# Kernel optimization log

Measured on AMD Instinct MI355X. Metric: run time of the kernel, lower is better.

## Reference

```python
import jax, jax.numpy as jnp
import numpy as np

N = 50000
V = 3
DIM = 128
H = 64


def setup_inputs() -> dict:
    key = jax.random.key(0)
    ks = jax.random.split(key, 8)
    x = jax.random.normal(ks[0], (N, V * DIM), dtype=jnp.float32)
    edge_index = jax.random.randint(ks[1], (2, 800000), 0, N, dtype=jnp.int64)
    Wv = jax.random.normal(ks[2], (V, DIM, H), dtype=jnp.float32) * (1.0 / np.sqrt(DIM))
    bv = jnp.zeros((V, H), dtype=jnp.float32)
    na_w = jax.random.normal(ks[3], (H, 1), dtype=jnp.float32) * (1.0 / np.sqrt(H))
    na_b = jnp.zeros((1,), dtype=jnp.float32)
    va_w1 = jax.random.normal(ks[4], (H, H // 2), dtype=jnp.float32) * (1.0 / np.sqrt(H))
    va_b1 = jnp.zeros((H // 2,), dtype=jnp.float32)
    va_w2 = jax.random.normal(ks[5], (H // 2, 1), dtype=jnp.float32) * (1.0 / np.sqrt(H // 2))
    va_b2 = jnp.zeros((1,), dtype=jnp.float32)
    cls_w = jax.random.normal(ks[6], (H, 2), dtype=jnp.float32) * (1.0 / np.sqrt(H))
    cls_b = jnp.zeros((2,), dtype=jnp.float32)
    return dict(x=x, edge_index=edge_index, Wv=Wv, bv=bv, na_w=na_w, na_b=na_b,
                va_w1=va_w1, va_b1=va_b1, va_w2=va_w2, va_b2=va_b2,
                cls_w=cls_w, cls_b=cls_b)


def reference(x, edge_index, Wv, bv, na_w, na_b, va_w1, va_b1, va_w2, va_b2, cls_w, cls_b):
    n = x.shape[0]
    # split into equal-dim views: [N, V, DIM]
    xv = x.reshape(n, V, DIM)

    # --- GCNConv (PyG defaults): linear transform, add self-loops, sym-norm aggregate, bias ---
    h = jnp.einsum('nvd,vdh->nvh', xv, Wv)  # [N, V, H]

    src = edge_index[0]
    dst = edge_index[1]
    loop = jnp.arange(n, dtype=src.dtype)
    src_full = jnp.concatenate([src, loop])
    dst_full = jnp.concatenate([dst, loop])

    ones = jnp.ones(src_full.shape[0], dtype=h.dtype)
    deg = jax.ops.segment_sum(ones, dst_full, num_segments=n)  # in-degree incl. self-loop
    dinv = jnp.where(deg > 0, 1.0 / jnp.sqrt(deg), 0.0)
    norm = dinv[src_full] * dinv[dst_full]  # [E+N]

    msgs = h[src_full] * norm[:, None, None]            # [E+N, V, H]
    agg = jax.ops.segment_sum(msgs, dst_full, num_segments=n)  # [N, V, H]
    agg = agg + bv[None, :, :]

    # ReLU
    emb = jax.nn.relu(agg)  # [N, V, H]

    # --- NodeAttentionLayer: softmax over nodes (dim=0), applied per view ---
    scores = jnp.einsum('nvh,ho->nvo', emb, na_w) + na_b  # [N, V, 1]
    att = jax.nn.softmax(scores, axis=0)
    emb_w = emb * att  # [N, V, H]

    # --- ViewAttention ---
    avg = jnp.mean(emb_w, axis=0)  # [V, H]
    vs = jnp.tanh(avg @ va_w1 + va_b1) @ va_w2 + va_b2  # [V, 1]
    vw = jax.nn.softmax(vs.T, axis=1)  # [1, V]
    fused = jnp.einsum('nvh,v->nh', emb_w, vw[0])  # [N, H]

    # --- classifier + log_softmax ---
    logits = fused @ cls_w + cls_b
    logp = jax.nn.log_softmax(logits, axis=1)
    return logp, fused, vw[0]
```

## Files before the change

### kernel.cpp

```cpp
#include <hip/hip_runtime.h>
#include <math.h>

#define NV 3
#define DIMX 128
#define HD 64
#define NVH 192
#define NBLK 256
#define NBUK 128
#define BSH 9

typedef unsigned int uint32;
typedef unsigned short ushort16;
typedef unsigned char uchar;
typedef __attribute__((ext_vector_type(8))) short short8;
typedef __attribute__((ext_vector_type(4))) float f32x4;

__device__ __forceinline__ unsigned fkey(float f){
  unsigned b = __float_as_uint(f);
  return (b & 0x80000000u) ? ~b : (b | 0x80000000u);
}
__device__ __forceinline__ float unkey(unsigned k){
  return __uint_as_float((k & 0x80000000u) ? (k ^ 0x80000000u) : ~k);
}
__device__ __forceinline__ uint32 bf16rne(float f){
  uint32 u = __float_as_uint(f);
  return (u + 0x7fffu + ((u >> 16) & 1u)) >> 16;
}
__device__ __forceinline__ float bfus(uint32 q){ return __uint_as_float(q << 16); }

__global__ void k_zero(float* __restrict__ wsum, float* __restrict__ sumexp, unsigned* __restrict__ maxkey){
  int t = threadIdx.x;
  if (t < NVH) wsum[t] = 0.f;
  else if (t < NVH+3) sumexp[t-NVH] = 0.f;
  else if (t < NVH+6) maxkey[t-NVH-3] = 0u;
}

__global__ __launch_bounds__(256) void k_hist(const int* __restrict__ ei, int E, int EPB,
                                              int* __restrict__ histT){
  __shared__ int sh[NBUK];
  int t = threadIdx.x, b = blockIdx.x;
  if (t < NBUK) sh[t] = 0;
  __syncthreads();
  int e0 = b*EPB, e1 = min(e0 + EPB, E);
  for (int i = e0 + t; i < e1; i += 256){
    int d = ei[E + i];
    atomicAdd(&sh[d >> BSH], 1);
  }
  __syncthreads();
  if (t < NBUK) histT[t*NBLK + b] = sh[t];
}

__global__ __launch_bounds__(1024) void k_hscan(int* __restrict__ histT){
  __shared__ int sh[1024];
  int t = threadIdx.x;
  int lo = t*32;
  int vals[32]; int s = 0;
  #pragma unroll
  for (int k = 0; k < 32; ++k){ vals[k] = histT[lo+k]; s += vals[k]; }
  sh[t] = s; __syncthreads();
  for (int ofs = 1; ofs < 1024; ofs <<= 1){
    int v = (t >= ofs) ? sh[t-ofs] : 0;
    __syncthreads();
    sh[t] += v;
    __syncthreads();
  }
  int run = sh[t] - s;
  #pragma unroll
  for (int k = 0; k < 32; ++k){ histT[lo+k] = run; run += vals[k]; }
}

__global__ __launch_bounds__(256) void k_scatter(const int* __restrict__ ei, int E, int EPB,
                                                 const int* __restrict__ ofsT, uint32* __restrict__ ebuf){
  __shared__ int cur[NBUK];
  int t = threadIdx.x, b = blockIdx.x;
  if (t < NBUK) cur[t] = ofsT[t*NBLK + b];
  __syncthreads();
  int e0 = b*EPB, e1 = min(e0 + EPB, E);
  for (int i = e0 + t; i < e1; i += 256){
    int s = ei[i], d = ei[E + i];
    int pos = atomicAdd(&cur[d >> BSH], 1);
    ebuf[pos] = ((uint32)(d & 511) << 16) | (uint32)s;
  }
}

__global__ __launch_bounds__(512) void k_csr(const uint32* __restrict__ ebuf, const int* __restrict__ ofsT,
                                             int E, int N, int* __restrict__ rowstart,
                                             float* __restrict__ dinv, int* __restrict__ csr){
  __shared__ int cnt[512];
  __shared__ int pre[512];
  int t = threadIdx.x, b = blockIdx.x;
  int estart = ofsT[b*NBLK];
  int eend   = ((b+1)*NBLK < NBUK*NBLK) ? ofsT[(b+1)*NBLK] : E;
  int n0 = b << BSH;
  int nn = min(512, N - n0);
  cnt[t] = 0;
  __syncthreads();
  for (int i = estart + t; i < eend; i += 512){
    atomicAdd(&cnt[ebuf[i] >> 16], 1);
  }
  __syncthreads();
  int c = cnt[t];
  pre[t] = c;
  __syncthreads();
  for (int ofs = 1; ofs < 512; ofs <<= 1){
    int v = (t >= ofs) ? pre[t-ofs] : 0;
    __syncthreads();
    pre[t] += v;
    __syncthreads();
  }
  int excl = pre[t] - c;
  if (t < nn){
    rowstart[n0 + t] = estart + excl;
    dinv[n0 + t] = rsqrtf((float)(c + 1));
  }
  if (b == gridDim.x - 1 && t == 0) rowstart[N] = E;
  cnt[t] = estart + excl;
  __syncthreads();
  for (int i = estart + t; i < eend; i += 512){
    uint32 e = ebuf[i];
    int pos = atomicAdd(&cnt[e >> 16], 1);
    csr[pos] = (int)(e & 0xFFFFu);
  }
}

__global__ __launch_bounds__(256) void k_wpack(const float* __restrict__ Wv, uint32* __restrict__ Wb){
  int t = blockIdx.x*blockDim.x + threadIdx.x;
  if (t >= 3072) return;
  int l = t & 63, s = (t >> 6) & 3, c = (t >> 8) & 3, v = t >> 10;
  int h = c*16 + (l & 15);
  int kbase = s*32 + (l >> 4)*8;
  const float* wp = Wv + v*8192 + h;
  uint32 o[4];
  #pragma unroll
  for (int jj = 0; jj < 4; ++jj){
    uint32 lo = bf16rne(wp[(kbase + 2*jj    )*64]);
    uint32 hi = bf16rne(wp[(kbase + 2*jj + 1)*64]);
    o[jj] = lo | (hi << 16);
  }
  Wb[t*4+0] = o[0]; Wb[t*4+1] = o[1]; Wb[t*4+2] = o[2]; Wb[t*4+3] = o[3];
}

__global__ __launch_bounds__(256) void k_h(const float* __restrict__ x, const uint32* __restrict__ Wb,
                                           const float* __restrict__ dinv,
                                           uint32* __restrict__ hq32, float* __restrict__ scaleV,
                                           int N, int NT){
  int wv = (blockIdx.x*blockDim.x + threadIdx.x) >> 6;
  int lane = threadIdx.x & 63;
  int tile = wv / 3;
  int v = wv - tile*3;
  if (tile >= NT) return;
  int jrow = lane & 15;
  int kq   = lane >> 4;
  int nrow = tile*16 + jrow;
  const float* xr = x + (size_t)nrow*384 + v*128 + kq*8;
  const short8* WB = (const short8*)Wb;

  f32x4 acc[4] = {};
  #pragma unroll
  for (int s = 0; s < 4; ++s){
    const float* p = xr + s*32;
    float4 f = *(const float4*)p, g = *(const float4*)(p+4);
    short8 a;
    a[0]=(short)bf16rne(f.x); a[1]=(short)bf16rne(f.y); a[2]=(short)bf16rne(f.z); a[3]=(short)bf16rne(f.w);
    a[4]=(short)bf16rne(g.x); a[5]=(short)bf16rne(g.y); a[6]=(short)bf16rne(g.z); a[7]=(short)bf16rne(g.w);
    #pragma unroll
    for (int c = 0; c < 4; ++c){
      short8 b = WB[(v*4 + c)*256 + s*64 + lane];
      acc[c] = __builtin_amdgcn_mfma_f32_16x16x32_bf16(a, b, acc[c], 0, 0, 0);
    }
  }

  float vv[4][4];
  float mx = 0.f;
  #pragma unroll
  for (int r = 0; r < 4; ++r){
    int n = tile*16 + kq*4 + r;
    float dv = dinv[n];
    #pragma unroll
    for (int c = 0; c < 4; ++c){
      float t = acc[c][r]*dv;
      vv[c][r] = t;
      mx = fmaxf(mx, fabsf(t));
    }
  }
  #pragma unroll
  for (int ofs = 1; ofs < 64; ofs <<= 1) mx = fmaxf(mx, __shfl_xor(mx, ofs));
  float inv = (mx > 0.f) ? 127.0f/mx : 0.f;
  #pragma unroll
  for (int r = 0; r < 4; ++r){
    int n = tile*16 + kq*4 + r;
    uint32 w = 0;
    #pragma unroll
    for (int c = 0; c < 4; ++c){
      uint32 q = (uint32)(int)(vv[c][r]*inv + 128.5f);
      w |= q << (8*c);
    }
    hq32[(size_t)n*48 + v*16 + jrow] = w;
  }
  if (lane == 0) scaleV[v*NT + tile] = mx * (1.0f/127.0f);
}

__global__ __launch_bounds__(256) void k_aggv(const uchar* __restrict__ hq, const float* __restrict__ scaleV,
                                              const int* __restrict__ rowstart, const int* __restrict__ csr,
                                              const float* __restrict__ dinv, const float* __restrict__ bv,
                                              const float* __restrict__ na_w, const float* __restrict__ na_b,
                                              ushort16* __restrict__ emb, float* __restrict__ scores,
                                              int N, int NT){
  int wid = (blockIdx.x*blockDim.x + threadIdx.x) >> 6;
  int lane = threadIdx.x & 63;
  if (wid >= N) return;
  int n = wid;
  int hp = (lane & 3)*16 + (lane >> 2);
  const uchar* hb = hq + (size_t)n*192;
  float q0 = (float)hb[lane], q1 = (float)hb[64+lane], q2 = (float)hb[128+lane];
  int grp = n >> 4;
  float c0 = scaleV[grp], c1 = scaleV[NT+grp], c2 = scaleV[2*NT+grp];
  float a0 = c0*q0, a1 = c1*q1, a2 = c2*q2;
  float ss0 = c0, ss1 = c1, ss2 = c2;
  int r0 = rowstart[n], r1 = rowstart[n+1];
  for (int base = r0; base < r1; base += 64){
    int m = r1 - base; if (m > 64) m = 64;
    int sv = (lane < m) ? __builtin_nontemporal_load(&csr[base + lane]) : 0;
    for (int i = 0; i < m; ++i){
      int s = __shfl(sv, i);
      const uchar* hs = hq + (size_t)s*192;
      float b0 = (float)hs[lane];
      float b1 = (float)hs[64+lane];
      float b2 = (float)hs[128+lane];
      int g2 = s >> 4;
      float d0 = scaleV[g2], d1 = scaleV[NT+g2], d2 = scaleV[2*NT+g2];
      a0 = fmaf(d0, b0, a0); ss0 += d0;
      a1 = fmaf(d1, b1, a1); ss1 += d1;
      a2 = fmaf(d2, b2, a2); ss2 += d2;
    }
  }
  a0 -= 128.0f*ss0;
  a1 -= 128.0f*ss1;
  a2 -= 128.0f*ss2;
  float dv = dinv[n];
  float e0 = fmaxf(a0*dv + bv[hp],      0.f);
  float e1 = fmaxf(a1*dv + bv[64+hp],   0.f);
  float e2 = fmaxf(a2*dv + bv[128+hp],  0.f);
  ushort16* ep = emb + (size_t)n*NVH;
  __builtin_nontemporal_store((ushort16)bf16rne(e0), &ep[hp]);
  __builtin_nontemporal_store((ushort16)bf16rne(e1), &ep[64+hp]);
  __builtin_nontemporal_store((ushort16)bf16rne(e2), &ep[128+hp]);
  float w = na_w[hp];
  float s0 = e0*w, s1 = e1*w, s2 = e2*w;
  #pragma unroll
  for (int ofs = 32; ofs >= 1; ofs >>= 1){
    s0 += __shfl_xor(s0, ofs);
    s1 += __shfl_xor(s1, ofs);
    s2 += __shfl_xor(s2, ofs);
  }
  if (lane == 0){
    float nb = na_b[0];
    scores[n] = s0 + nb; scores[N + n] = s1 + nb; scores[2*N + n] = s2 + nb;
  }
}

__global__ void k_max(const float* __restrict__ scores, int N, unsigned* __restrict__ maxkey){
  __shared__ float sh[256];
  int v = blockIdx.y;
  const float* sp = scores + (size_t)v*N;
  int base = blockIdx.x*2048 + threadIdx.x;
  float m = -3.0e38f;
  #pragma unroll
  for (int k = 0; k < 8; ++k){
    int i = base + k*256;
    if (i < N) m = fmaxf(m, sp[i]);
  }
  sh[threadIdx.x] = m; __syncthreads();
  for (int ofs = 128; ofs >= 1; ofs >>= 1){
    if (threadIdx.x < ofs) sh[threadIdx.x] = fmaxf(sh[threadIdx.x], sh[threadIdx.x+ofs]);
    __syncthreads();
  }
  if (threadIdx.x == 0) atomicMax(&maxkey[v], fkey(sh[0]));
}

__global__ __launch_bounds__(256) void k_wsum(const ushort16* __restrict__ emb, const float* __restrict__ scores,
                                              const unsigned* __restrict__ maxkey, float* __restrict__ wsum,
                                              float* __restrict__ sumexp, int N){
  __shared__ float shw[4][NVH];
  __shared__ float shse[4][4];
  int t = threadIdx.x;
  int lane = t & 63;
  int wv = t >> 6;
  int gw = (blockIdx.x*blockDim.x + t) >> 6;
  int nw = (gridDim.x*blockDim.x) >> 6;
  float m0 = unkey(maxkey[0]), m1 = unkey(maxkey[1]), m2 = unkey(maxkey[2]);
  float w0=0.f, w1=0.f, w2=0.f, se0=0.f, se1=0.f, se2=0.f;
  for (int n = gw; n < N; n += nw){
    const ushort16* ep = emb + (size_t)n*NVH;
    float x0 = expf(scores[n]       - m0);
    float x1 = expf(scores[N + n]   - m1);
    float x2 = expf(scores[2*N + n] - m2);
    w0 += bfus(ep[lane])*x0; w1 += bfus(ep[64+lane])*x1; w2 += bfus(ep[128+lane])*x2;
    se0 += x0; se1 += x1; se2 += x2;
  }
  shw[wv][lane]     = w0;
  shw[wv][64+lane]  = w1;
  shw[wv][128+lane] = w2;
  #pragma unroll
  for (int ofs = 32; ofs >= 1; ofs >>= 1){
    se0 += __shfl_xor(se0, ofs);
    se1 += __shfl_xor(se1, ofs);
    se2 += __shfl_xor(se2, ofs);
  }
  if (lane == 0){ shse[wv][0] = se0; shse[wv][1] = se1; shse[wv][2] = se2; }
  __syncthreads();
  if (t < NVH){
    float s = shw[0][t] + shw[1][t] + shw[2][t] + shw[3][t];
    atomicAdd(&wsum[t], s);
  } else if (t >= NVH && t < NVH+3){
    int v = t - NVH;
    float s = shse[0][v] + shse[1][v] + shse[2][v] + shse[3][v];
    atomicAdd(&sumexp[v], s);
  }
}

__global__ __launch_bounds__(64) void k_view(const float* __restrict__ wsum, const float* __restrict__ sumexp,
                                             const float* __restrict__ va_w1, const float* __restrict__ va_b1,
                                             const float* __restrict__ va_w2, const float* __restrict__ va_b2,
                                             float* __restrict__ g, float* __restrict__ out_vw, int N){
  __shared__ float avg[NV][64];
  __shared__ float z1[NV][32];
  int t = threadIdx.x;
  if (t < 64){
    for (int v = 0; v < NV; ++v) avg[v][t] = wsum[v*64+t] / (sumexp[v] * (float)N);
  }
  __syncthreads();
  if (t < 32){
    for (int v = 0; v < NV; ++v){
      float a = va_b1[t];
      for (int h = 0; h < 64; ++h) a += avg[v][h]*va_w1[h*32 + t];
      z1[v][t] = tanhf(a);
    }
  }
  __syncthreads();
  if (t == 0){
    float vs[NV];
    for (int v = 0; v < NV; ++v){
      float a = va_b2[0];
      for (int j = 0; j < 32; ++j) a += z1[v][j]*va_w2[j];
      vs[v] = a;
    }
    float m = fmaxf(vs[0], fmaxf(vs[1], vs[2]));
    float e0 = expf(vs[0]-m), e1 = expf(vs[1]-m), e2 = expf(vs[2]-m);
    float inv = 1.f/(e0+e1+e2);
    float vw0 = e0*inv, vw1 = e1*inv, vw2 = e2*inv;
    out_vw[0] = vw0; out_vw[1] = vw1; out_vw[2] = vw2;
    g[0] = vw0/sumexp[0]; g[1] = vw1/sumexp[1]; g[2] = vw2/sumexp[2];
  }
}

__global__ __launch_bounds__(256) void k_fused(const ushort16* __restrict__ emb, const float* __restrict__ scores,
                                               const unsigned* __restrict__ maxkey, const float* __restrict__ g,
                                               const float* __restrict__ cls_w, const float* __restrict__ cls_b,
                                               float* __restrict__ out, int N){
  int wid = (blockIdx.x*blockDim.x + threadIdx.x) >> 6;
  int lane = threadIdx.x & 63;
  if (wid >= N) return;
  int n = wid;
  float m0 = unkey(maxkey[0]), m1 = unkey(maxkey[1]), m2 = unkey(maxkey[2]);
  float w0 = expf(scores[n]       - m0)*g[0];
  float w1 = expf(scores[N + n]   - m1)*g[1];
  float w2 = expf(scores[2*N + n] - m2)*g[2];
  const ushort16* ep = emb + (size_t)n*NVH;
  float fu = bfus(ep[lane])*w0 + bfus(ep[64+lane])*w1 + bfus(ep[128+lane])*w2;
  out[(size_t)2*N + (size_t)n*64 + lane] = fu;
  float c0 = fu*cls_w[lane*2 + 0];
  float c1 = fu*cls_w[lane*2 + 1];
  #pragma unroll
  for (int ofs = 32; ofs >= 1; ofs >>= 1){
    c0 += __shfl_xor(c0, ofs);
    c1 += __shfl_xor(c1, ofs);
  }
  if (lane == 0){
    float l0 = c0 + cls_b[0], l1 = c1 + cls_b[1];
    float m = fmaxf(l0, l1);
    float lse = m + logf(expf(l0-m) + expf(l1-m));
    out[(size_t)n*2]     = l0 - lse;
    out[(size_t)n*2 + 1] = l1 - lse;
  }
}

extern "C" void kernel_launch(void* const* d_in, const int* in_sizes, int n_in,
                              void* d_out, int out_size, void* d_ws, size_t ws_size,
                              hipStream_t stream){
  const float* x     = (const float*)d_in[0];
  const int*   ei    = (const int*)d_in[1];
  const float* Wv    = (const float*)d_in[2];
  const float* bv    = (const float*)d_in[3];
  const float* na_w  = (const float*)d_in[4];
  const float* na_b  = (const float*)d_in[5];
  const float* va_w1 = (const float*)d_in[6];
  const float* va_b1 = (const float*)d_in[7];
  const float* va_w2 = (const float*)d_in[8];
  const float* va_b2 = (const float*)d_in[9];
  const float* cls_w = (const float*)d_in[10];
  const float* cls_b = (const float*)d_in[11];
  int N = in_sizes[0] / (NV*DIMX);
  int E = in_sizes[1] / 2;
  float* out = (float*)d_out;
  int NT = (N + 15) / 16;

  char* wptr = (char*)d_ws;
  size_t off = 0;
  auto alloc = [&](size_t bytes){ void* p = wptr + off; off += (bytes + 255) & ~255ull; return p; };
  uint32*    hq       = (uint32*)alloc((size_t)N*48*4);
  float*     scaleV   = (float*)alloc((size_t)3*NT*4);
  ushort16*  emb      = (ushort16*)alloc((size_t)N*NVH*2);
  int*       csr      = (int*)alloc((size_t)E*4);
  uint32*    ebuf     = (uint32*)alloc((size_t)E*4);
  int*       histT    = (int*)alloc((size_t)NBUK*NBLK*4);
  int*       rowstart = (int*)alloc((size_t)(N+1)*4);
  float*     dinv     = (float*)alloc((size_t)N*4);
  float*     scores   = (float*)alloc((size_t)3*N*4);
  unsigned*  maxkey   = (unsigned*)alloc(3*4);
  float*     sumexp   = (float*)alloc(3*4);
  float*     wsum     = (float*)alloc(192*4);
  float*     g        = (float*)alloc(3*4);
  uint32*    Wb       = (uint32*)alloc(3072*16);

  int EPB = (E + NBLK - 1) / NBLK;
  int nbuck = (N + 511) >> BSH;
  k_zero   <<<1, 256, 0, stream>>>(wsum, sumexp, maxkey);
  k_hist   <<<NBLK, 256, 0, stream>>>(ei, E, EPB, histT);
  k_hscan  <<<1, 1024, 0, stream>>>(histT);
  k_scatter<<<NBLK, 256, 0, stream>>>(ei, E, EPB, histT, ebuf);
  k_csr    <<<nbuck, 512, 0, stream>>>(ebuf, histT, E, N, rowstart, dinv, csr);
  k_wpack  <<<12, 256, 0, stream>>>(Wv, Wb);
  int hwaves = NT*3;
  k_h      <<<(hwaves*64+255)/256, 256, 0, stream>>>(x, Wb, dinv, hq, scaleV, N, NT);
  k_aggv   <<<(N*64+255)/256, 256, 0, stream>>>((const uchar*)hq, scaleV, rowstart, csr, dinv, bv,
                                                na_w, na_b, emb, scores, N, NT);
  dim3 gm((N+2047)/2048, NV);
  k_max    <<<gm, 256, 0, stream>>>(scores, N, maxkey);
  k_wsum   <<<304, 256, 0, stream>>>(emb, scores, maxkey, wsum, sumexp, N);
  k_view   <<<1, 64, 0, stream>>>(wsum, sumexp, va_w1, va_b1, va_w2, va_b2, g,
                                  out + (size_t)2*N + (size_t)N*64, N);
  k_fused  <<<(N*64+255)/256, 256, 0, stream>>>(emb, scores, maxkey, g, cls_w, cls_b, out, N);
}
```

Before: 184.5 us.

## Interleave quantized views per hidden unit and unroll neighbor gather by four

The int8 quantized h table changes from three view-major 64-byte blocks per node to one 256-byte row. Each hidden unit gets a 4-byte word holding the three views plus padding, and the per-tile scales are stored as a float4. The aggregation kernel now does one 32-bit load and one float4 scale load per neighbor instead of three byte loads and three scale loads. It also unrolls the neighbor loop by four to put more gathers in flight. The trade-off is that the row grows from 192 to 256 bytes, so each gather moves about a third more bytes, and k_h now writes single bytes scattered across the row.

```diff
diff --git a/kernel.cpp b/kernel.cpp
--- a/kernel.cpp
+++ b/kernel.cpp
@@ -27,6 +27,9 @@
   return (u + 0x7fffu + ((u >> 16) & 1u)) >> 16;
 }
 __device__ __forceinline__ float bfus(uint32 q){ return __uint_as_float(q << 16); }
+__device__ __forceinline__ float ub0(uint32 p){ return (float)(p & 0xffu); }
+__device__ __forceinline__ float ub1(uint32 p){ return (float)((p >> 8) & 0xffu); }
+__device__ __forceinline__ float ub2(uint32 p){ return (float)((p >> 16) & 0xffu); }
 
 __global__ void k_zero(float* __restrict__ wsum, float* __restrict__ sumexp, unsigned* __restrict__ maxkey){
   int t = threadIdx.x;
@@ -142,7 +145,7 @@
 
 __global__ __launch_bounds__(256) void k_h(const float* __restrict__ x, const uint32* __restrict__ Wb,
                                            const float* __restrict__ dinv,
-                                           uint32* __restrict__ hq32, float* __restrict__ scaleV,
+                                           uchar* __restrict__ hq8, float* __restrict__ scale4,
                                            int N, int NT){
   int wv = (blockIdx.x*blockDim.x + threadIdx.x) >> 6;
   int lane = threadIdx.x & 63;
@@ -189,63 +192,71 @@
   #pragma unroll
   for (int r = 0; r < 4; ++r){
     int n = tile*16 + kq*4 + r;
-    uint32 w = 0;
     #pragma unroll
     for (int c = 0; c < 4; ++c){
       uint32 q = (uint32)(int)(vv[c][r]*inv + 128.5f);
-      w |= q << (8*c);
-    }
-    hq32[(size_t)n*48 + v*16 + jrow] = w;
-  }
-  if (lane == 0) scaleV[v*NT + tile] = mx * (1.0f/127.0f);
-}
-
-__global__ __launch_bounds__(256) void k_aggv(const uchar* __restrict__ hq, const float* __restrict__ scaleV,
+      hq8[(size_t)n*256 + (c*16 + jrow)*4 + v] = (uchar)q;
+    }
+  }
+  if (lane == 0) scale4[tile*4 + v] = mx * (1.0f/127.0f);
+}
+
+__global__ __launch_bounds__(256) void k_aggv(const uint32* __restrict__ hq4, const float4* __restrict__ sc4,
                                               const int* __restrict__ rowstart, const int* __restrict__ csr,
                                               const float* __restrict__ dinv, const float* __restrict__ bv,
                                               const float* __restrict__ na_w, const float* __restrict__ na_b,
-                                              ushort16* __restrict__ emb, float* __restrict__ scores,
-                                              int N, int NT){
+                                              ushort16* __restrict__ emb, float* __restrict__ scores, int N){
   int wid = (blockIdx.x*blockDim.x + threadIdx.x) >> 6;
   int lane = threadIdx.x & 63;
   if (wid >= N) return;
   int n = wid;
-  int hp = (lane & 3)*16 + (lane >> 2);
-  const uchar* hb = hq + (size_t)n*192;
-  float q0 = (float)hb[lane], q1 = (float)hb[64+lane], q2 = (float)hb[128+lane];
-  int grp = n >> 4;
-  float c0 = scaleV[grp], c1 = scaleV[NT+grp], c2 = scaleV[2*NT+grp];
-  float a0 = c0*q0, a1 = c1*q1, a2 = c2*q2;
-  float ss0 = c0, ss1 = c1, ss2 = c2;
+  uint32 ps = hq4[(size_t)n*64 + lane];
+  float4 cs = sc4[n >> 4];
+  float a0 = cs.x*ub0(ps), a1 = cs.y*ub1(ps), a2 = cs.z*ub2(ps);
+  float ss0 = cs.x, ss1 = cs.y, ss2 = cs.z;
   int r0 = rowstart[n], r1 = rowstart[n+1];
   for (int base = r0; base < r1; base += 64){
     int m = r1 - base; if (m > 64) m = 64;
     int sv = (lane < m) ? __builtin_nontemporal_load(&csr[base + lane]) : 0;
-    for (int i = 0; i < m; ++i){
+    int i = 0;
+    for (; i + 3 < m; i += 4){
+      int s0 = __shfl(sv, i), s1 = __shfl(sv, i+1), s2 = __shfl(sv, i+2), s3 = __shfl(sv, i+3);
+      uint32 p0 = hq4[(size_t)s0*64 + lane];
+      uint32 p1 = hq4[(size_t)s1*64 + lane];
+      uint32 p2 = hq4[(size_t)s2*64 + lane];
+      uint32 p3 = hq4[(size_t)s3*64 + lane];
+      float4 f0 = sc4[s0 >> 4];
+      float4 f1 = sc4[s1 >> 4];
+      float4 f2 = sc4[s2 >> 4];
+      float4 f3 = sc4[s3 >> 4];
+      a0 = fmaf(f0.x, ub0(p0), a0); a1 = fmaf(f0.y, ub1(p0), a1); a2 = fmaf(f0.z, ub2(p0), a2);
+      a0 = fmaf(f1.x, ub0(p1), a0); a1 = fmaf(f1.y, ub1(p1), a1); a2 = fmaf(f1.z, ub2(p1), a2);
+      a0 = fmaf(f2.x, ub0(p2), a0); a1 = fmaf(f2.y, ub1(p2), a1); a2 = fmaf(f2.z, ub2(p2), a2);
+      a0 = fmaf(f3.x, ub0(p3), a0); a1 = fmaf(f3.y, ub1(p3), a1); a2 = fmaf(f3.z, ub2(p3), a2);
+      ss0 += f0.x + f1.x + f2.x + f3.x;
+      ss1 += f0.y + f1.y + f2.y + f3.y;
+      ss2 += f0.z + f1.z + f2.z + f3.z;
+    }
+    for (; i < m; ++i){
       int s = __shfl(sv, i);
-      const uchar* hs = hq + (size_t)s*192;
-      float b0 = (float)hs[lane];
-      float b1 = (float)hs[64+lane];
-      float b2 = (float)hs[128+lane];
-      int g2 = s >> 4;
-      float d0 = scaleV[g2], d1 = scaleV[NT+g2], d2 = scaleV[2*NT+g2];
-      a0 = fmaf(d0, b0, a0); ss0 += d0;
-      a1 = fmaf(d1, b1, a1); ss1 += d1;
-      a2 = fmaf(d2, b2, a2); ss2 += d2;
+      uint32 p = hq4[(size_t)s*64 + lane];
+      float4 f = sc4[s >> 4];
+      a0 = fmaf(f.x, ub0(p), a0); a1 = fmaf(f.y, ub1(p), a1); a2 = fmaf(f.z, ub2(p), a2);
+      ss0 += f.x; ss1 += f.y; ss2 += f.z;
     }
   }
   a0 -= 128.0f*ss0;
   a1 -= 128.0f*ss1;
   a2 -= 128.0f*ss2;
   float dv = dinv[n];
-  float e0 = fmaxf(a0*dv + bv[hp],      0.f);
-  float e1 = fmaxf(a1*dv + bv[64+hp],   0.f);
-  float e2 = fmaxf(a2*dv + bv[128+hp],  0.f);
+  float e0 = fmaxf(a0*dv + bv[lane],      0.f);
+  float e1 = fmaxf(a1*dv + bv[64+lane],   0.f);
+  float e2 = fmaxf(a2*dv + bv[128+lane],  0.f);
   ushort16* ep = emb + (size_t)n*NVH;
-  __builtin_nontemporal_store((ushort16)bf16rne(e0), &ep[hp]);
-  __builtin_nontemporal_store((ushort16)bf16rne(e1), &ep[64+hp]);
-  __builtin_nontemporal_store((ushort16)bf16rne(e2), &ep[128+hp]);
-  float w = na_w[hp];
+  __builtin_nontemporal_store((ushort16)bf16rne(e0), &ep[lane]);
+  __builtin_nontemporal_store((ushort16)bf16rne(e1), &ep[64+lane]);
+  __builtin_nontemporal_store((ushort16)bf16rne(e2), &ep[128+lane]);
+  float w = na_w[lane];
   float s0 = e0*w, s1 = e1*w, s2 = e2*w;
   #pragma unroll
   for (int ofs = 32; ofs >= 1; ofs >>= 1){
@@ -408,8 +419,8 @@
   char* wptr = (char*)d_ws;
   size_t off = 0;
   auto alloc = [&](size_t bytes){ void* p = wptr + off; off += (bytes + 255) & ~255ull; return p; };
-  uint32*    hq       = (uint32*)alloc((size_t)N*48*4);
-  float*     scaleV   = (float*)alloc((size_t)3*NT*4);
+  uchar*     hq       = (uchar*)alloc((size_t)N*256);
+  float*     scale4   = (float*)alloc((size_t)NT*4*4);
   ushort16*  emb      = (ushort16*)alloc((size_t)N*NVH*2);
   int*       csr      = (int*)alloc((size_t)E*4);
   uint32*    ebuf     = (uint32*)alloc((size_t)E*4);
@@ -432,9 +443,9 @@
   k_csr    <<<nbuck, 512, 0, stream>>>(ebuf, histT, E, N, rowstart, dinv, csr);
   k_wpack  <<<12, 256, 0, stream>>>(Wv, Wb);
   int hwaves = NT*3;
-  k_h      <<<(hwaves*64+255)/256, 256, 0, stream>>>(x, Wb, dinv, hq, scaleV, N, NT);
-  k_aggv   <<<(N*64+255)/256, 256, 0, stream>>>((const uchar*)hq, scaleV, rowstart, csr, dinv, bv,
-                                                na_w, na_b, emb, scores, N, NT);
+  k_h      <<<(hwaves*64+255)/256, 256, 0, stream>>>(x, Wb, dinv, hq, scale4, N, NT);
+  k_aggv   <<<(N*64+255)/256, 256, 0, stream>>>((const uint32*)hq, (const float4*)scale4, rowstart, csr,
+                                                dinv, bv, na_w, na_b, emb, scores, N);
   dim3 gm((N+2047)/2048, NV);
   k_max    <<<gm, 256, 0, stream>>>(scores, N, maxkey);
   k_wsum   <<<304, 256, 0, stream>>>(emb, scores, maxkey, wsum, sumexp, N);
```

Result: faster. 164.5 us (-10.8%).
